# Kernel tuning notes

Hardware: AMD Instinct MI355X
Metric: run time of the kernel (lower is better)

## Reference

```python
import jax, jax.numpy as jnp
import numpy as np

# ---- static config (mirrors TritonMoEConfig) ----
N_EMBD = 1024
EXPERT_SIZES = [(4, 1024), (4, 2048)]  # (count, width) pairs
TOP_K = 2                              # num_active_experts
B, S = 1, 2048

WIDTHS = []
for count, size in EXPERT_SIZES:
    WIDTHS += [size] * count
OFFSETS = np.concatenate([[0], np.cumsum(WIDTHS)]).astype(np.int64)
E = len(WIDTHS)                 # 8 experts
TOTAL_W = int(OFFSETS[-1])      # 12288
MAX_W = max(WIDTHS)             # 2048


def setup_inputs() -> dict:
    key = jax.random.key(0)
    k1, k2, k3, k4 = jax.random.split(key, 4)
    x = jax.random.normal(k1, (B, S, N_EMBD), jnp.float32)
    # router: nn.Linear(n_embd, num_experts, bias=False) -> weight [E, d]
    router_w = jax.random.normal(k2, (E, N_EMBD), jnp.float32) * 0.02
    # trunc_normal(std=0.02, a=-0.06, b=0.06) == truncated_normal(-3,3)*0.02
    w1 = jax.random.truncated_normal(k3, -3.0, 3.0, (N_EMBD, TOTAL_W), jnp.float32) * 0.02
    w2 = jax.random.truncated_normal(k4, -3.0, 3.0, (TOTAL_W, N_EMBD), jnp.float32) * 0.02
    return {"x": x, "router_w": router_w, "w1": w1, "w2": w2}


def _stack_experts(w1, w2):
    # Slice the flat concatenated weights into per-expert blocks, zero-padded
    # to MAX_W. Zero pad is exact: relu(x@0)^2 == 0 and padded w2 rows are 0.
    W1e, W2e = [], []
    for e in range(E):  # fixed small loop over structurally distinct experts
        off, wd = int(OFFSETS[e]), WIDTHS[e]
        pad = MAX_W - wd
        W1e.append(jnp.pad(w1[:, off:off + wd], ((0, 0), (0, pad))))
        W2e.append(jnp.pad(w2[off:off + wd, :], ((0, pad), (0, 0))))
    return jnp.stack(W1e), jnp.stack(W2e)  # [E,d,maxw], [E,maxw,d]


def reference(x, router_w, w1, w2):
    b, s, d = x.shape
    xf = x.reshape(-1, d)  # [T, d]
    # routing: sigmoid probs (fp32), top-k, renormalize
    logits = xf @ router_w.T  # [T, E]
    probs = jax.nn.sigmoid(logits.astype(jnp.float32))
    topw, sel = jax.lax.top_k(probs, TOP_K)  # [T, K]
    topw = topw / (topw.sum(-1, keepdims=True) + 1e-20)
    topw = topw.astype(x.dtype)
    # combine[t, e] = sum_k topw[t,k] * (sel[t,k] == e)
    onehot = (sel[:, :, None] == jnp.arange(E)[None, None, :])
    combine = jnp.sum(topw[:, :, None] * onehot, axis=1)  # [T, E]
    # expert MLP with relu_squared activation; combine zeros unselected experts
    W1e, W2e = _stack_experts(w1, w2)
    h = jnp.einsum('td,edw->tew', xf, W1e)   # up-proj, [T,E,maxw]
    h = jnp.square(jax.nn.relu(h))           # relu_squared
    y = jnp.einsum('tew,ewd->ted', h, W2e)   # down-proj, [T,E,d]
    out = jnp.einsum('ted,te->td', y, combine)
    return out.reshape(b, s, d)
```

## Files before the change

### kernel.cpp

```cpp
#include <hip/hip_runtime.h>
#include <hip/hip_bf16.h>

#define T_TOKENS 2048
#define D_EMBD   1024
#define N_EXP    8
#define TOTAL_W  12288
#define CAP      2048
#define CAPH     2048

typedef __attribute__((ext_vector_type(8))) short bf16x8;
typedef __attribute__((ext_vector_type(4))) float f32x4;
typedef __attribute__((ext_vector_type(4))) unsigned short u16x4;
typedef __attribute__((ext_vector_type(8))) unsigned short u16x8;

__device__ __constant__ int d_OFF[N_EXP] = {0,1024,2048,3072,4096,6144,8192,10240};
__device__ __constant__ int d_WID[N_EXP] = {1024,1024,1024,1024,2048,2048,2048,2048};

#define WS_TOK   1024
#define WS_SLK   (WS_TOK + N_EXP*CAP*4)
#define WS_WGT   (WS_SLK + N_EXP*CAP*4)
#define WS_WG2   (WS_WGT + N_EXP*CAP*4)
#define WS_XB    (WS_WG2 + T_TOKENS*2*4)
#define WS_W1B   (WS_XB + T_TOKENS*D_EMBD*2)
#define WS_W2B   (WS_W1B + D_EMBD*TOTAL_W*2)
#define WS_H     (WS_W2B + (size_t)TOTAL_W*D_EMBD*2)
#define WS_END   (WS_H + (size_t)TOTAL_W*CAPH*2)
#define WS_Y     WS_XB

__device__ __forceinline__ void gload_lds16(const void* g, void* l) {
    __builtin_amdgcn_global_load_lds(
        (const __attribute__((address_space(1))) void*)g,
        (__attribute__((address_space(3))) void*)l, 16, 0, 0);
}

__device__ __forceinline__ unsigned short f2bf(float f) {
    __hip_bfloat16 h = __float2bfloat16(f);
    return *reinterpret_cast<unsigned short*>(&h);
}

__global__ __launch_bounds__(64) void zero_kernel(int* __restrict__ cnt) {
    if (threadIdx.x < N_EXP) cnt[threadIdx.x << 5] = 0;
}

__device__ __forceinline__ void router_body(
    int rb, int tid, char* smem,
    const float* __restrict__ x, const float* __restrict__ rw,
    int* __restrict__ cnt, int* __restrict__ tok, int* __restrict__ slotk,
    float* __restrict__ wgtl, float* __restrict__ wgt2)
{
    int*   lcnt  = (int*)smem;
    int*   lbase = (int*)(smem + 32);
    int   (*ltok)[32] = (int(*)[32])(smem + 64);
    float (*lwgt)[32] = (float(*)[32])(smem + 64 + 1024);
    int   (*lkk)[32]  = (int(*)[32])(smem + 64 + 2048);

    const int wv = tid >> 6, lane = tid & 63;
    if (tid < N_EXP) lcnt[tid] = 0;
    __syncthreads();

    const float4* x4  = (const float4*)x;
    const float4* rw4 = (const float4*)rw;
    for (int ts = 0; ts < 8; ++ts) {
        const int t = rb * 32 + wv * 8 + ts;
        float4 xv[4];
#pragma unroll
        for (int i = 0; i < 4; ++i) xv[i] = x4[(size_t)t * 256 + lane + 64 * i];
        float acc[N_EXP];
#pragma unroll
        for (int e = 0; e < N_EXP; ++e) {
            float a = 0.f;
#pragma unroll
            for (int i = 0; i < 4; ++i) {
                float4 w4 = rw4[e * 256 + lane + 64 * i];
                a += xv[i].x * w4.x + xv[i].y * w4.y + xv[i].z * w4.z + xv[i].w * w4.w;
            }
            acc[e] = a;
        }
#pragma unroll
        for (int e = 0; e < N_EXP; ++e)
#pragma unroll
            for (int o = 32; o > 0; o >>= 1) acc[e] += __shfl_xor(acc[e], o, 64);

        if (lane == 0) {
            float p[N_EXP];
#pragma unroll
            for (int e = 0; e < N_EXP; ++e) p[e] = 1.f / (1.f + __expf(-acc[e]));
            int e0 = 0;
#pragma unroll
            for (int e = 1; e < N_EXP; ++e) if (p[e] > p[e0]) e0 = e;
            int e1 = (e0 == 0) ? 1 : 0;
#pragma unroll
            for (int e = 0; e < N_EXP; ++e) if (e != e0 && p[e] > p[e1]) e1 = e;
            float w0 = p[e0], w1 = p[e1], s = w0 + w1 + 1e-20f;
            int s0 = atomicAdd(&lcnt[e0], 1);
            ltok[e0][s0] = t;  lwgt[e0][s0] = w0 / s;  lkk[e0][s0] = 0;
            int s1 = atomicAdd(&lcnt[e1], 1);
            ltok[e1][s1] = t;  lwgt[e1][s1] = w1 / s;  lkk[e1][s1] = 1;
        }
    }
    __syncthreads();
    if (tid < N_EXP) lbase[tid] = atomicAdd(&cnt[tid << 5], lcnt[tid]);
    __syncthreads();
    {
        const int e = tid >> 5, i = tid & 31;
        if (i < lcnt[e]) {
            int dst = e * CAP + lbase[e] + i;
            int t   = ltok[e][i], k = lkk[e][i];
            tok[dst]   = t;
            wgtl[dst]  = lwgt[e][i];
            slotk[dst] = t * 2 + k;
            wgt2[t * 2 + k] = lwgt[e][i];
        }
    }
}

__device__ __forceinline__ void transpose_body(
    const float* __restrict__ in, __hip_bfloat16* __restrict__ out,
    int R, int C, int br, int bc, int tid, char* smem)
{
    float (*ls)[65] = (float(*)[65])smem;
    const int r0 = br << 6, c0 = bc << 6;
#pragma unroll
    for (int i = 0; i < 4; ++i) {
        int flat = i * 1024 + tid * 4;
        int r = flat >> 6, c = flat & 63;
        float4 v = *reinterpret_cast<const float4*>(&in[(size_t)(r0 + r) * C + c0 + c]);
        ls[r][c] = v.x; ls[r][c + 1] = v.y; ls[r][c + 2] = v.z; ls[r][c + 3] = v.w;
    }
    __syncthreads();
#pragma unroll
    for (int i = 0; i < 2; ++i) {
        int flat = i * 2048 + tid * 8;
        int cc = flat >> 6, rr = flat & 63;
        u16x8 o;
#pragma unroll
        for (int q = 0; q < 8; ++q) o[q] = f2bf(ls[rr + q][cc]);
        *reinterpret_cast<u16x8*>(&out[(size_t)(c0 + cc) * R + r0 + rr]) = o;
    }
}

__global__ __launch_bounds__(256) void prep2_kernel(
    const float* __restrict__ x, const float* __restrict__ rw,
    const float* __restrict__ w1, const float* __restrict__ w2,
    int* __restrict__ cnt, int* __restrict__ tok, int* __restrict__ slotk,
    float* __restrict__ wgtl, float* __restrict__ wgt2,
    __hip_bfloat16* __restrict__ xb, __hip_bfloat16* __restrict__ w1b,
    __hip_bfloat16* __restrict__ w2b)
{
    __shared__ __align__(16) char smem[16640];
    const int bx = blockIdx.x, tid = threadIdx.x;
    if (bx < 64) {
        router_body(bx, tid, smem, x, rw, cnt, tok, slotk, wgtl, wgt2);
    } else if (bx < 1088) {
        int i4 = (bx - 64) * 512 + tid * 2;
        const float4 v0 = reinterpret_cast<const float4*>(x)[i4];
        const float4 v1 = reinterpret_cast<const float4*>(x)[i4 + 1];
        u16x8 o;
        o[0] = f2bf(v0.x); o[1] = f2bf(v0.y); o[2] = f2bf(v0.z); o[3] = f2bf(v0.w);
        o[4] = f2bf(v1.x); o[5] = f2bf(v1.y); o[6] = f2bf(v1.z); o[7] = f2bf(v1.w);
        *reinterpret_cast<u16x8*>(xb + (size_t)i4 * 4) = o;
    } else if (bx < 4160) {
        int tb = bx - 1088;
        transpose_body(w1, w1b, D_EMBD, TOTAL_W, tb / 192, tb % 192, tid, smem);
    } else {
        int tb = bx - 4160;
        transpose_body(w2, w2b, TOTAL_W, D_EMBD, tb / 16, tb % 16, tid, smem);
    }
}

__global__ __launch_bounds__(256) void router2_kernel(
    const float* __restrict__ x, const float* __restrict__ rw,
    int* __restrict__ cnt, int* __restrict__ tok, int* __restrict__ slotk,
    float* __restrict__ wgtl, float* __restrict__ wgt2)
{
    __shared__ __align__(16) char smem[16640];
    router_body(blockIdx.x, threadIdx.x, smem, x, rw, cnt, tok, slotk, wgtl, wgt2);
}

__global__ __launch_bounds__(256) void gemm1_kernel(
    const char* __restrict__ xb, const char* __restrict__ w1b,
    const int* __restrict__ cnt, const int* __restrict__ tok,
    __hip_bfloat16* __restrict__ H)
{
    int bx0 = blockIdx.x;
    int bx = (bx0 & 7) * 384 + (bx0 >> 3);
    int e, tt, nT;
    if (bx < 2048) {
        e = 4 + (bx >> 9); int r = bx & 511; tt = r >> 4; nT = r & 15;
    } else {
        int b2 = bx - 2048; e = b2 >> 8; int r = b2 & 255; tt = r >> 3; nT = r & 7;
    }
    const int nt = cnt[e << 5];
    if (tt * 64 >= nt) return;

    const int we  = d_WID[e];
    const int n0  = nT * 128;
    const int tid = threadIdx.x;
    const int wv  = tid >> 6, lane = tid & 63;
    const int wr  = wv >> 1, wc = wv & 1;

    __shared__ __align__(16) char lds[2][24576];
    __shared__ int ts_s[64];

    if (tid < 64) {
        int s = tt * 64 + tid;
        ts_s[tid] = (s < nt) ? tok[e * CAP + s] : 0;
    }
    __syncthreads();

    f32x4 acc[2][4];
#pragma unroll
    for (int mi = 0; mi < 2; ++mi)
#pragma unroll
        for (int nj = 0; nj < 4; ++nj) acc[mi][nj] = (f32x4){0.f,0.f,0.f,0.f};

    const char* w1row = w1b + (size_t)(d_OFF[e] + n0) * 2048;

    auto STAGE = [&](int buf, int ks) {
        const int k0b = ks * 128;
#pragma unroll
        for (int j = 0; j < 6; ++j) {
            const int flat = j * 4096 + tid * 16;
            char* dst = lds[buf] + flat;
            if (flat < 8192) {
                int r = flat >> 7, cb = flat & 127;
                gload_lds16(xb + (size_t)ts_s[r] * 2048 + k0b + (cb ^ ((r & 7) << 4)), dst);
            } else {
                int f2 = flat - 8192, n = f2 >> 7, cb = f2 & 127;
                gload_lds16(w1row + (size_t)n * 2048 + k0b + (cb ^ ((n & 7) << 4)), dst);
            }
        }
    };
    auto COMPUTE = [&](int buf) {
        const char* LA = lds[buf];
        const char* LB = lds[buf] + 8192;
#pragma unroll
        for (int ksl = 0; ksl < 2; ++ksl) {
            const int kb = ksl * 64 + (lane >> 4) * 16;
            bf16x8 a[2], b[4];
#pragma unroll
            for (int mi = 0; mi < 2; ++mi) {
                int row = wr * 32 + mi * 16 + (lane & 15);
                a[mi] = *(const bf16x8*)(LA + row * 128 + (kb ^ ((row & 7) << 4)));
            }
#pragma unroll
            for (int nj = 0; nj < 4; ++nj) {
                int n = wc * 64 + nj * 16 + (lane & 15);
                b[nj] = *(const bf16x8*)(LB + n * 128 + (kb ^ ((n & 7) << 4)));
            }
#pragma unroll
            for (int mi = 0; mi < 2; ++mi)
#pragma unroll
                for (int nj = 0; nj < 4; ++nj)
                    acc[mi][nj] = __builtin_amdgcn_mfma_f32_16x16x32_bf16(
                        a[mi], b[nj], acc[mi][nj], 0, 0, 0);
        }
    };

    STAGE(0, 0);
    int cur = 0;
    for (int ks = 0; ks < 16; ++ks) {
        if (ks + 1 < 16) {
            STAGE(cur ^ 1, ks + 1);
            asm volatile("s_waitcnt vmcnt(6)" ::: "memory");
        } else {
            asm volatile("s_waitcnt vmcnt(0)" ::: "memory");
        }
        __builtin_amdgcn_s_barrier();
        __builtin_amdgcn_sched_barrier(0);
        COMPUTE(cur);
        __builtin_amdgcn_sched_barrier(0);
        __builtin_amdgcn_s_barrier();
        cur ^= 1;
    }

    const size_t hbase = (size_t)d_OFF[e] * CAPH;
#pragma unroll
    for (int mi = 0; mi < 2; ++mi)
#pragma unroll
        for (int q = 0; q < 4; ++q) {
            int row  = wr * 32 + mi * 16 + (lane >> 4) * 4 + q;
            int slot = tt * 64 + row;
            __hip_bfloat16* hp = H + hbase + (size_t)slot * we + n0 + wc * 64 + (lane & 15);
#pragma unroll
            for (int nj = 0; nj < 4; ++nj) {
                float v = fmaxf(acc[mi][nj][q], 0.f);
                hp[nj * 16] = __float2bfloat16(v * v);
            }
        }
}

__global__ __launch_bounds__(256) void gemm2_kernel(
    const char* __restrict__ Hb, const char* __restrict__ w2b,
    const int* __restrict__ cnt, const int* __restrict__ slotk,
    float* __restrict__ Y)
{
    int bx0 = blockIdx.x;
    int bx = (bx0 & 7) * 256 + (bx0 >> 3);
    int e, tt, nT;
    if (bx < 1024) {
        e = 4 + (bx >> 8); int r = bx & 255; tt = r >> 3; nT = r & 7;
    } else {
        int b2 = bx - 1024; e = b2 >> 8; int r = b2 & 255; tt = r >> 3; nT = r & 7;
    }
    const int nt = cnt[e << 5];
    if (tt * 64 >= nt) return;

    const int we  = d_WID[e];
    const int n0  = nT * 128;
    const int tid = threadIdx.x;
    const int wv  = tid >> 6, lane = tid & 63;
    const int wr  = wv >> 1, wc = wv & 1;

    __shared__ __align__(16) char lds[2][24576];
    __shared__ int yk_s[64];

    if (tid < 64) {
        int s = tt * 64 + tid;
        yk_s[tid] = (s < nt) ? slotk[e * CAP + s] : 0;
    }
    __syncthreads();

    f32x4 acc[2][4];
#pragma unroll
    for (int mi = 0; mi < 2; ++mi)
#pragma unroll
        for (int nj = 0; nj < 4; ++nj) acc[mi][nj] = (f32x4){0.f,0.f,0.f,0.f};

    const char* Habase = Hb + ((size_t)d_OFF[e] * CAPH + (size_t)tt * 64 * we) * 2;
    const char* w2base = w2b + ((size_t)n0 * TOTAL_W + d_OFF[e]) * 2;
    const int   ksteps = we >> 6;

    auto STAGE = [&](int buf, int ks) {
        const int k0b = ks * 128;
#pragma unroll
        for (int j = 0; j < 6; ++j) {
            const int flat = j * 4096 + tid * 16;
            char* dst = lds[buf] + flat;
            if (flat < 8192) {
                int r = flat >> 7, cb = flat & 127;
                gload_lds16(Habase + (size_t)r * (we * 2) + k0b + (cb ^ ((r & 7) << 4)), dst);
            } else {
                int f2 = flat - 8192, n = f2 >> 7, cb = f2 & 127;
                gload_lds16(w2base + (size_t)n * (TOTAL_W * 2) + k0b + (cb ^ ((n & 7) << 4)), dst);
            }
        }
    };
    auto COMPUTE = [&](int buf) {
        const char* LA = lds[buf];
        const char* LB = lds[buf] + 8192;
#pragma unroll
        for (int ksl = 0; ksl < 2; ++ksl) {
            const int kb = ksl * 64 + (lane >> 4) * 16;
            bf16x8 a[2], b[4];
#pragma unroll
            for (int mi = 0; mi < 2; ++mi) {
                int row = wr * 32 + mi * 16 + (lane & 15);
                a[mi] = *(const bf16x8*)(LA + row * 128 + (kb ^ ((row & 7) << 4)));
            }
#pragma unroll
            for (int nj = 0; nj < 4; ++nj) {
                int n = wc * 64 + nj * 16 + (lane & 15);
                b[nj] = *(const bf16x8*)(LB + n * 128 + (kb ^ ((n & 7) << 4)));
            }
#pragma unroll
            for (int mi = 0; mi < 2; ++mi)
#pragma unroll
                for (int nj = 0; nj < 4; ++nj)
                    acc[mi][nj] = __builtin_amdgcn_mfma_f32_16x16x32_bf16(
                        a[mi], b[nj], acc[mi][nj], 0, 0, 0);
        }
    };

    STAGE(0, 0);
    int cur = 0;
    for (int ks = 0; ks < ksteps; ++ks) {
        if (ks + 1 < ksteps) {
            STAGE(cur ^ 1, ks + 1);
            asm volatile("s_waitcnt vmcnt(6)" ::: "memory");
        } else {
            asm volatile("s_waitcnt vmcnt(0)" ::: "memory");
        }
        __builtin_amdgcn_s_barrier();
        __builtin_amdgcn_sched_barrier(0);
        COMPUTE(cur);
        __builtin_amdgcn_sched_barrier(0);
        __builtin_amdgcn_s_barrier();
        cur ^= 1;
    }

#pragma unroll
    for (int mi = 0; mi < 2; ++mi)
#pragma unroll
        for (int q = 0; q < 4; ++q) {
            int row  = wr * 32 + mi * 16 + (lane >> 4) * 4 + q;
            int slot = tt * 64 + row;
            if (slot < nt) {
                float* yp = Y + (size_t)yk_s[row] * D_EMBD + n0 + wc * 64 + (lane & 15);
#pragma unroll
                for (int nj = 0; nj < 4; ++nj)
                    yp[nj * 16] = acc[mi][nj][q];
            }
        }
}

__global__ __launch_bounds__(256) void gather_kernel(
    const float* __restrict__ Y, const float* __restrict__ wgt2,
    float* __restrict__ out)
{
    const int t = blockIdx.x, tid = threadIdx.x;
    const float w0 = wgt2[t * 2], w1 = wgt2[t * 2 + 1];
    const float4 y0 = reinterpret_cast<const float4*>(Y + (size_t)(t * 2) * D_EMBD)[tid];
    const float4 y1 = reinterpret_cast<const float4*>(Y + (size_t)(t * 2 + 1) * D_EMBD)[tid];
    float4 o;
    o.x = w0 * y0.x + w1 * y1.x;  o.y = w0 * y0.y + w1 * y1.y;
    o.z = w0 * y0.z + w1 * y1.z;  o.w = w0 * y0.w + w1 * y1.w;
    reinterpret_cast<float4*>(out + (size_t)t * D_EMBD)[tid] = o;
}

__global__ __launch_bounds__(256, 3) void moe_group_kernel(
    const float* __restrict__ x, const float* __restrict__ w1,
    const float* __restrict__ w2, const int* __restrict__ cnt,
    const int* __restrict__ tok, const float* __restrict__ wgtl,
    float* __restrict__ out)
{
    int e, tt, colh, wh, nwh;
    int bx = blockIdx.x;
    if (bx < 1024) { e = bx >> 8; int rem = bx & 255; wh = rem & 1; colh = (rem >> 1) & 1; tt = rem >> 2; nwh = 2; }
    else { int b2 = bx - 1024; e = 4 + (b2 >> 9); int rem = b2 & 511; wh = rem & 3; colh = (rem >> 2) & 1; tt = rem >> 3; nwh = 4; }
    const int nt = cnt[e << 5];
    if (tt * 32 >= nt) return;

    const int tid = threadIdx.x;
    const int off = d_OFF[e];
    const int wtn = d_WID[e] >> 7;
    const int wpb = wtn / nwh;
    const int wt0 = wh * wpb;

    __shared__ float xs[128][36];
    __shared__ float hs[128][36];
    __shared__ int   ts_s[32];
    __shared__ float wg_s[32];

    if (tid < 32) {
        int s = tt * 32 + tid;
        ts_s[tid] = (s < nt) ? tok[e * CAP + s] : 0;
        wg_s[tid] = (s < nt) ? wgtl[e * CAP + s] : 0.f;
    }

    const int tg = tid >> 5, cg = tid & 31;
    float acc_dn[4][16];
#pragma unroll
    for (int a = 0; a < 4; ++a)
#pragma unroll
        for (int m = 0; m < 16; ++m) acc_dn[a][m] = 0.f;

    for (int wt = wt0; wt < wt0 + wpb; ++wt) {
        float au[4][4];
#pragma unroll
        for (int a = 0; a < 4; ++a)
#pragma unroll
            for (int b = 0; b < 4; ++b) au[a][b] = 0.f;
        const int cw1 = off + wt * 128 + cg * 4;
        for (int dc = 0; dc < 8; ++dc) {
            const int d0 = dc * 128;
            __syncthreads();
#pragma unroll
            for (int r = 0; r < 16; ++r) {
                int flat = r * 256 + tid, ii = flat & 127, t = flat >> 7;
                xs[ii][t] = x[(size_t)ts_s[t] * D_EMBD + d0 + ii];
            }
            __syncthreads();
            const float* pw = w1 + (size_t)d0 * TOTAL_W + cw1;
            for (int ii = 0; ii < 128; ++ii) {
                const float4 xv = *reinterpret_cast<const float4*>(&xs[ii][tg * 4]);
                const float4 wv = *reinterpret_cast<const float4*>(pw);
                pw += TOTAL_W;
                const float xa[4] = {xv.x, xv.y, xv.z, xv.w};
                const float wb[4] = {wv.x, wv.y, wv.z, wv.w};
#pragma unroll
                for (int a = 0; a < 4; ++a)
#pragma unroll
                    for (int b = 0; b < 4; ++b) au[a][b] += xa[a] * wb[b];
            }
        }
#pragma unroll
        for (int b = 0; b < 4; ++b) {
            float4 v;
            float r0 = fmaxf(au[0][b], 0.f), r1 = fmaxf(au[1][b], 0.f);
            float r2 = fmaxf(au[2][b], 0.f), r3 = fmaxf(au[3][b], 0.f);
            v.x = r0 * r0; v.y = r1 * r1; v.z = r2 * r2; v.w = r3 * r3;
            *reinterpret_cast<float4*>(&hs[cg * 4 + b][tg * 4]) = v;
        }
        __syncthreads();
        const float* pw2 = w2 + (size_t)(off + wt * 128) * D_EMBD + colh * 512 + cg * 4;
        for (int j = 0; j < 128; ++j) {
            const float4 hv = *reinterpret_cast<const float4*>(&hs[j][tg * 4]);
            const float ha[4] = {hv.x, hv.y, hv.z, hv.w};
            const float* row = pw2 + (size_t)j * D_EMBD;
#pragma unroll
            for (int b = 0; b < 4; ++b) {
                const float4 wv = *reinterpret_cast<const float4*>(row + b * 128);
                const float wq[4] = {wv.x, wv.y, wv.z, wv.w};
#pragma unroll
                for (int a = 0; a < 4; ++a)
#pragma unroll
                    for (int q = 0; q < 4; ++q)
                        acc_dn[a][b * 4 + q] += ha[a] * wq[q];
            }
        }
        __syncthreads();
    }
#pragma unroll
    for (int a = 0; a < 4; ++a) {
        const int   t  = ts_s[tg * 4 + a];
        const float wg = wg_s[tg * 4 + a];
        float* ot = out + (size_t)t * D_EMBD + colh * 512 + cg * 4;
#pragma unroll
        for (int b = 0; b < 4; ++b)
#pragma unroll
            for (int q = 0; q < 4; ++q)
                atomicAdd(&ot[b * 128 + q], wg * acc_dn[a][b * 4 + q]);
    }
}

extern "C" void kernel_launch(void* const* d_in, const int* in_sizes, int n_in,
                              void* d_out, int out_size, void* d_ws, size_t ws_size,
                              hipStream_t stream) {
    const float* x  = (const float*)d_in[0];
    const float* rw = (const float*)d_in[1];
    const float* w1 = (const float*)d_in[2];
    const float* w2 = (const float*)d_in[3];
    float* out = (float*)d_out;

    char*  ws    = (char*)d_ws;
    int*   cnt   = (int*)ws;
    int*   tokl  = (int*)(ws + WS_TOK);
    int*   slotk = (int*)(ws + WS_SLK);
    float* wgtl  = (float*)(ws + WS_WGT);
    float* wgt2  = (float*)(ws + WS_WG2);

    if (ws_size >= WS_END) {
        __hip_bfloat16* xb  = (__hip_bfloat16*)(ws + WS_XB);
        __hip_bfloat16* w1b = (__hip_bfloat16*)(ws + WS_W1B);
        __hip_bfloat16* w2b = (__hip_bfloat16*)(ws + WS_W2B);
        __hip_bfloat16* H   = (__hip_bfloat16*)(ws + WS_H);
        float*          Y   = (float*)(ws + WS_Y);

        zero_kernel<<<1, 64, 0, stream>>>(cnt);
        prep2_kernel<<<7232, 256, 0, stream>>>(x, rw, w1, w2, cnt, tokl, slotk, wgtl, wgt2,
                                               xb, w1b, w2b);
        gemm1_kernel<<<3072, 256, 0, stream>>>((const char*)xb, (const char*)w1b, cnt, tokl, H);
        gemm2_kernel<<<2048, 256, 0, stream>>>((const char*)H, (const char*)w2b, cnt, slotk, Y);
        gather_kernel<<<T_TOKENS, 256, 0, stream>>>(Y, wgt2, out);
    } else {
        hipMemsetAsync(d_ws, 0, 1024, stream);
        hipMemsetAsync(d_out, 0, (size_t)out_size * sizeof(float), stream);
        router2_kernel<<<T_TOKENS / 32, 256, 0, stream>>>(x, rw, cnt, tokl, slotk, wgtl, wgt2);
        moe_group_kernel<<<1024 + 2048, 256, 0, stream>>>(x, w1, w2, cnt, tokl, wgtl, out);
    }
}
```

Measured before the change: 100.5 us.

## Fuse fp32 weight conversion into GEMM B-tile loading, drop transpose prep

Removes the separate pass that transposed w1/w2 to bf16 in workspace. Both GEMMs now load fp32 weight columns straight into registers, convert them to bf16 and write the swizzled tiles into LDS, with register prefetch pipelined across k-steps. This avoids writing and re-reading about 50MB of converted weights. In exchange each GEMM block reads fp32 weights (twice the bytes), re-reads them once per token tile, and adds conversion ALU work and register pressure inside the main loop.

```diff
diff --git a/kernel.cpp b/kernel.cpp
--- a/kernel.cpp
+++ b/kernel.cpp
@@ -114,44 +114,17 @@
     }
 }
 
-__device__ __forceinline__ void transpose_body(
-    const float* __restrict__ in, __hip_bfloat16* __restrict__ out,
-    int R, int C, int br, int bc, int tid, char* smem)
-{
-    float (*ls)[65] = (float(*)[65])smem;
-    const int r0 = br << 6, c0 = bc << 6;
-#pragma unroll
-    for (int i = 0; i < 4; ++i) {
-        int flat = i * 1024 + tid * 4;
-        int r = flat >> 6, c = flat & 63;
-        float4 v = *reinterpret_cast<const float4*>(&in[(size_t)(r0 + r) * C + c0 + c]);
-        ls[r][c] = v.x; ls[r][c + 1] = v.y; ls[r][c + 2] = v.z; ls[r][c + 3] = v.w;
-    }
-    __syncthreads();
-#pragma unroll
-    for (int i = 0; i < 2; ++i) {
-        int flat = i * 2048 + tid * 8;
-        int cc = flat >> 6, rr = flat & 63;
-        u16x8 o;
-#pragma unroll
-        for (int q = 0; q < 8; ++q) o[q] = f2bf(ls[rr + q][cc]);
-        *reinterpret_cast<u16x8*>(&out[(size_t)(c0 + cc) * R + r0 + rr]) = o;
-    }
-}
-
-__global__ __launch_bounds__(256) void prep2_kernel(
+__global__ __launch_bounds__(256) void prep7_kernel(
     const float* __restrict__ x, const float* __restrict__ rw,
-    const float* __restrict__ w1, const float* __restrict__ w2,
     int* __restrict__ cnt, int* __restrict__ tok, int* __restrict__ slotk,
     float* __restrict__ wgtl, float* __restrict__ wgt2,
-    __hip_bfloat16* __restrict__ xb, __hip_bfloat16* __restrict__ w1b,
-    __hip_bfloat16* __restrict__ w2b)
+    __hip_bfloat16* __restrict__ xb)
 {
     __shared__ __align__(16) char smem[16640];
     const int bx = blockIdx.x, tid = threadIdx.x;
     if (bx < 64) {
         router_body(bx, tid, smem, x, rw, cnt, tok, slotk, wgtl, wgt2);
-    } else if (bx < 1088) {
+    } else {
         int i4 = (bx - 64) * 512 + tid * 2;
         const float4 v0 = reinterpret_cast<const float4*>(x)[i4];
         const float4 v1 = reinterpret_cast<const float4*>(x)[i4 + 1];
@@ -159,12 +132,6 @@
         o[0] = f2bf(v0.x); o[1] = f2bf(v0.y); o[2] = f2bf(v0.z); o[3] = f2bf(v0.w);
         o[4] = f2bf(v1.x); o[5] = f2bf(v1.y); o[6] = f2bf(v1.z); o[7] = f2bf(v1.w);
         *reinterpret_cast<u16x8*>(xb + (size_t)i4 * 4) = o;
-    } else if (bx < 4160) {
-        int tb = bx - 1088;
-        transpose_body(w1, w1b, D_EMBD, TOTAL_W, tb / 192, tb % 192, tid, smem);
-    } else {
-        int tb = bx - 4160;
-        transpose_body(w2, w2b, TOTAL_W, D_EMBD, tb / 16, tb % 16, tid, smem);
     }
 }
 
@@ -178,7 +145,7 @@
 }
 
 __global__ __launch_bounds__(256) void gemm1_kernel(
-    const char* __restrict__ xb, const char* __restrict__ w1b,
+    const char* __restrict__ xb, const float* __restrict__ w1,
     const int* __restrict__ cnt, const int* __restrict__ tok,
     __hip_bfloat16* __restrict__ H)
 {
@@ -214,21 +181,40 @@
 #pragma unroll
         for (int nj = 0; nj < 4; ++nj) acc[mi][nj] = (f32x4){0.f,0.f,0.f,0.f};
 
-    const char* w1row = w1b + (size_t)(d_OFF[e] + n0) * 2048;
-
-    auto STAGE = [&](int buf, int ks) {
+    const float* bcol = w1 + d_OFF[e] + n0 + (tid & 63) * 2;
+    const int koT = (tid >> 6) * 8;
+
+    float2 br[2][8];
+
+    auto B_LOAD = [&](int ks) {
+#pragma unroll
+        for (int ph = 0; ph < 2; ++ph) {
+            const int kb = ks * 64 + ph * 32 + koT;
+#pragma unroll
+            for (int j = 0; j < 8; ++j)
+                br[ph][j] = *reinterpret_cast<const float2*>(bcol + (size_t)(kb + j) * TOTAL_W);
+        }
+    };
+    auto B_WRITE = [&](int buf) {
+        char* LB = lds[buf] + 8192;
+#pragma unroll
+        for (int ph = 0; ph < 2; ++ph) {
+            const int ko = ph * 32 + koT;
+            const int n  = (tid & 63) * 2;
+            u16x8 p0, p1;
+#pragma unroll
+            for (int j = 0; j < 8; ++j) { p0[j] = f2bf(br[ph][j].x); p1[j] = f2bf(br[ph][j].y); }
+            *reinterpret_cast<u16x8*>(LB + n * 128 + ((ko * 2) ^ ((n & 7) << 4))) = p0;
+            *reinterpret_cast<u16x8*>(LB + (n + 1) * 128 + ((ko * 2) ^ (((n + 1) & 7) << 4))) = p1;
+        }
+    };
+    auto A_STAGE = [&](int buf, int ks) {
         const int k0b = ks * 128;
 #pragma unroll
-        for (int j = 0; j < 6; ++j) {
+        for (int j = 0; j < 2; ++j) {
             const int flat = j * 4096 + tid * 16;
-            char* dst = lds[buf] + flat;
-            if (flat < 8192) {
-                int r = flat >> 7, cb = flat & 127;
-                gload_lds16(xb + (size_t)ts_s[r] * 2048 + k0b + (cb ^ ((r & 7) << 4)), dst);
-            } else {
-                int f2 = flat - 8192, n = f2 >> 7, cb = f2 & 127;
-                gload_lds16(w1row + (size_t)n * 2048 + k0b + (cb ^ ((n & 7) << 4)), dst);
-            }
+            int r = flat >> 7, cb = flat & 127;
+            gload_lds16(xb + (size_t)ts_s[r] * 2048 + k0b + (cb ^ ((r & 7) << 4)), lds[buf] + flat);
         }
     };
     auto COMPUTE = [&](int buf) {
@@ -257,20 +243,28 @@
         }
     };
 
-    STAGE(0, 0);
+    B_LOAD(0); A_STAGE(0, 0);
+    asm volatile("s_waitcnt vmcnt(2)" ::: "memory");
+    B_WRITE(0);
+
     int cur = 0;
     for (int ks = 0; ks < 16; ++ks) {
         if (ks + 1 < 16) {
-            STAGE(cur ^ 1, ks + 1);
-            asm volatile("s_waitcnt vmcnt(6)" ::: "memory");
+            B_LOAD(ks + 1); A_STAGE(cur ^ 1, ks + 1);
+            asm volatile("s_waitcnt vmcnt(18)" ::: "memory");
         } else {
             asm volatile("s_waitcnt vmcnt(0)" ::: "memory");
         }
+        asm volatile("s_waitcnt lgkmcnt(0)" ::: "memory");
         __builtin_amdgcn_s_barrier();
         __builtin_amdgcn_sched_barrier(0);
         COMPUTE(cur);
         __builtin_amdgcn_sched_barrier(0);
         __builtin_amdgcn_s_barrier();
+        if (ks + 1 < 16) {
+            asm volatile("s_waitcnt vmcnt(2)" ::: "memory");
+            B_WRITE(cur ^ 1);
+        }
         cur ^= 1;
     }
 
@@ -291,7 +285,7 @@
 }
 
 __global__ __launch_bounds__(256) void gemm2_kernel(
-    const char* __restrict__ Hb, const char* __restrict__ w2b,
+    const char* __restrict__ Hb, const float* __restrict__ w2,
     const int* __restrict__ cnt, const int* __restrict__ slotk,
     float* __restrict__ Y)
 {
@@ -327,23 +321,42 @@
 #pragma unroll
         for (int nj = 0; nj < 4; ++nj) acc[mi][nj] = (f32x4){0.f,0.f,0.f,0.f};
 
-    const char* Habase = Hb + ((size_t)d_OFF[e] * CAPH + (size_t)tt * 64 * we) * 2;
-    const char* w2base = w2b + ((size_t)n0 * TOTAL_W + d_OFF[e]) * 2;
-    const int   ksteps = we >> 6;
-
-    auto STAGE = [&](int buf, int ks) {
+    const char*  Habase = Hb + ((size_t)d_OFF[e] * CAPH + (size_t)tt * 64 * we) * 2;
+    const float* bcol = w2 + (size_t)d_OFF[e] * D_EMBD + n0 + (tid & 63) * 2;
+    const int    koT = (tid >> 6) * 8;
+    const int    ksteps = we >> 6;
+
+    float2 br[2][8];
+
+    auto B_LOAD = [&](int ks) {
+#pragma unroll
+        for (int ph = 0; ph < 2; ++ph) {
+            const int kb = ks * 64 + ph * 32 + koT;
+#pragma unroll
+            for (int j = 0; j < 8; ++j)
+                br[ph][j] = *reinterpret_cast<const float2*>(bcol + (size_t)(kb + j) * D_EMBD);
+        }
+    };
+    auto B_WRITE = [&](int buf) {
+        char* LB = lds[buf] + 8192;
+#pragma unroll
+        for (int ph = 0; ph < 2; ++ph) {
+            const int ko = ph * 32 + koT;
+            const int n  = (tid & 63) * 2;
+            u16x8 p0, p1;
+#pragma unroll
+            for (int j = 0; j < 8; ++j) { p0[j] = f2bf(br[ph][j].x); p1[j] = f2bf(br[ph][j].y); }
+            *reinterpret_cast<u16x8*>(LB + n * 128 + ((ko * 2) ^ ((n & 7) << 4))) = p0;
+            *reinterpret_cast<u16x8*>(LB + (n + 1) * 128 + ((ko * 2) ^ (((n + 1) & 7) << 4))) = p1;
+        }
+    };
+    auto A_STAGE = [&](int buf, int ks) {
         const int k0b = ks * 128;
 #pragma unroll
-        for (int j = 0; j < 6; ++j) {
+        for (int j = 0; j < 2; ++j) {
             const int flat = j * 4096 + tid * 16;
-            char* dst = lds[buf] + flat;
-            if (flat < 8192) {
-                int r = flat >> 7, cb = flat & 127;
-                gload_lds16(Habase + (size_t)r * (we * 2) + k0b + (cb ^ ((r & 7) << 4)), dst);
-            } else {
-                int f2 = flat - 8192, n = f2 >> 7, cb = f2 & 127;
-                gload_lds16(w2base + (size_t)n * (TOTAL_W * 2) + k0b + (cb ^ ((n & 7) << 4)), dst);
-            }
+            int r = flat >> 7, cb = flat & 127;
+            gload_lds16(Habase + (size_t)r * (we * 2) + k0b + (cb ^ ((r & 7) << 4)), lds[buf] + flat);
         }
     };
     auto COMPUTE = [&](int buf) {
@@ -372,20 +385,28 @@
         }
     };
 
-    STAGE(0, 0);
+    B_LOAD(0); A_STAGE(0, 0);
+    asm volatile("s_waitcnt vmcnt(2)" ::: "memory");
+    B_WRITE(0);
+
     int cur = 0;
     for (int ks = 0; ks < ksteps; ++ks) {
         if (ks + 1 < ksteps) {
-            STAGE(cur ^ 1, ks + 1);
-            asm volatile("s_waitcnt vmcnt(6)" ::: "memory");
+            B_LOAD(ks + 1); A_STAGE(cur ^ 1, ks + 1);
+            asm volatile("s_waitcnt vmcnt(18)" ::: "memory");
         } else {
             asm volatile("s_waitcnt vmcnt(0)" ::: "memory");
         }
+        asm volatile("s_waitcnt lgkmcnt(0)" ::: "memory");
         __builtin_amdgcn_s_barrier();
         __builtin_amdgcn_sched_barrier(0);
         COMPUTE(cur);
         __builtin_amdgcn_sched_barrier(0);
         __builtin_amdgcn_s_barrier();
+        if (ks + 1 < ksteps) {
+            asm volatile("s_waitcnt vmcnt(2)" ::: "memory");
+            B_WRITE(cur ^ 1);
+        }
         cur ^= 1;
     }
 
@@ -542,16 +563,13 @@
 
     if (ws_size >= WS_END) {
         __hip_bfloat16* xb  = (__hip_bfloat16*)(ws + WS_XB);
-        __hip_bfloat16* w1b = (__hip_bfloat16*)(ws + WS_W1B);
-        __hip_bfloat16* w2b = (__hip_bfloat16*)(ws + WS_W2B);
         __hip_bfloat16* H   = (__hip_bfloat16*)(ws + WS_H);
         float*          Y   = (float*)(ws + WS_Y);
 
         zero_kernel<<<1, 64, 0, stream>>>(cnt);
-        prep2_kernel<<<7232, 256, 0, stream>>>(x, rw, w1, w2, cnt, tokl, slotk, wgtl, wgt2,
-                                               xb, w1b, w2b);
-        gemm1_kernel<<<3072, 256, 0, stream>>>((const char*)xb, (const char*)w1b, cnt, tokl, H);
-        gemm2_kernel<<<2048, 256, 0, stream>>>((const char*)H, (const char*)w2b, cnt, slotk, Y);
+        prep7_kernel<<<1088, 256, 0, stream>>>(x, rw, cnt, tokl, slotk, wgtl, wgt2, xb);
+        gemm1_kernel<<<3072, 256, 0, stream>>>((const char*)xb, w1, cnt, tokl, H);
+        gemm2_kernel<<<2048, 256, 0, stream>>>((const char*)H, w2, cnt, slotk, Y);
         gather_kernel<<<T_TOKENS, 256, 0, stream>>>(Y, wgt2, out);
     } else {
         hipMemsetAsync(d_ws, 0, 1024, stream);
```

Measured after the change: 160.5 us. 1.6x slower.
